# Kernel tuning notes

Measured on AMD Instinct MI355X. Metric: run time of the kernel, lower is better.

Reference implementation:

```python
import jax, jax.numpy as jnp
import numpy as np

N_NODES = 100000
N_EDGES = 1600000
IN_DIM = 64
OUT_DIM = 64
HIDDEN = 64  # fixed in edge_weight_mlp
POS_DIM = 3


def setup_inputs() -> dict:
    key = jax.random.key(0)
    ks = jax.random.split(key, 10)
    x = jax.random.normal(ks[0], (N_NODES, IN_DIM), dtype=jnp.float32)
    edge_index = jax.random.randint(ks[1], (2, N_EDGES), 0, N_NODES, dtype=jnp.int64)
    pos = jax.random.normal(ks[2], (N_NODES, POS_DIM), dtype=jnp.float32)
    # edge_weight_mlp params: Linear(2*IN_DIM+1 -> 64), Linear(64 -> 1)
    s1 = 1.0 / np.sqrt(2 * IN_DIM + 1)
    w1 = jax.random.uniform(ks[3], (2 * IN_DIM + 1, HIDDEN), jnp.float32, -s1, s1)
    b1 = jax.random.uniform(ks[4], (HIDDEN,), jnp.float32, -s1, s1)
    s2 = 1.0 / np.sqrt(HIDDEN)
    w2 = jax.random.uniform(ks[5], (HIDDEN, 1), jnp.float32, -s2, s2)
    b2 = jax.random.uniform(ks[6], (1,), jnp.float32, -s2, s2)
    # transform: Linear(IN_DIM -> OUT_DIM)
    st = 1.0 / np.sqrt(IN_DIM)
    wt = jax.random.uniform(ks[7], (IN_DIM, OUT_DIM), jnp.float32, -st, st)
    bt = jax.random.uniform(ks[8], (OUT_DIM,), jnp.float32, -st, st)
    return {"x": x, "edge_index": edge_index, "pos": pos,
            "w1": w1, "b1": b1, "w2": w2, "b2": b2, "wt": wt, "bt": bt}


def reference(x, edge_index, pos, w1, b1, w2, b2, wt, bt):
    src, dst = edge_index[0], edge_index[1]
    # edge weights: MLP on [x_src, x_dst, |pos_dst - pos_src|]
    edge_length = jnp.linalg.norm(pos[dst] - pos[src], axis=1, keepdims=True)  # [E,1]
    edge_feat = jnp.concatenate([x[src], x[dst], edge_length], axis=1)  # [E, 2*in+1]
    h = jax.nn.relu(edge_feat @ w1 + b1)
    edge_weights = jax.nn.sigmoid(h @ w2 + b2)  # [E,1]
    # node transform, gather, weight, scatter-add
    x_t = x @ wt + bt  # [N, out]
    messages = x_t[src] * edge_weights  # [E, out]
    out = jax.ops.segment_sum(messages, dst, num_segments=x.shape[0])  # [N, out]
    return out, edge_weights
```

## Files before the change

kernel.cpp:

```cpp
#include <hip/hip_runtime.h>
#include <hip/hip_bf16.h>
#include <math.h>

#define NN 100000
#define NE 1600000
#define CAP 48
#define NB 391
#define BCAP 4608
#define EPB 4096
#define NBLKA ((NE + EPB - 1) / EPB)
#define NPREP ((NN + 63) / 64)
#define PSTR 72

typedef __attribute__((ext_vector_type(8))) short short8;
typedef __attribute__((ext_vector_type(4))) float floatx4;

static __device__ __forceinline__ unsigned short f2bb(float f) {
    __hip_bfloat16 h = __float2bfloat16(f);
    return *(unsigned short*)&h;
}
static __device__ __forceinline__ float hi_f(unsigned u) {
    return __uint_as_float(u & 0xFFFF0000u);
}
static __device__ __forceinline__ float lo_f(unsigned u) {
    return __uint_as_float(u << 16);
}

__global__ __launch_bounds__(256) void fused_prep_bucket(
    const float* __restrict__ x, const float* __restrict__ w1,
    const float* __restrict__ b1, const float* __restrict__ pos,
    const int* __restrict__ ei,
    unsigned int* __restrict__ rec, unsigned short* __restrict__ hd,
    float4* __restrict__ pos4, int* __restrict__ gcursor,
    uint2* __restrict__ bucketed) {
    __shared__ __align__(16) unsigned char smem[(64 + 128) * PSTR * 2];
    int t = threadIdx.x;
    if (blockIdx.x < NPREP) {
        unsigned short* As = (unsigned short*)smem;
        unsigned short* Bs = As + 64 * PSTR;
        int nbase = blockIdx.x * 64;
        {
            int r = t & 63;
            int node = nbase + r; if (node >= NN) node = NN - 1;
            const float4* xr = (const float4*)(x + (size_t)node * 64);
#pragma unroll
            for (int i = 0; i < 4; ++i) {
                int s = (t >> 6) + 4 * i;
                float4 v = xr[s];
                ushort4 o = {f2bb(v.x), f2bb(v.y), f2bb(v.z), f2bb(v.w)};
                *(ushort4*)&As[r * PSTR + s * 4] = o;
            }
        }
        {
            int n = t & 127;
            int kh = t >> 7;
            int krow = (n < 64) ? 0 : 64;
            int col = n & 63;
#pragma unroll
            for (int i = 0; i < 32; ++i) {
                int k = kh * 32 + i;
                Bs[n * PSTR + k] = f2bb(w1[(krow + k) * 64 + col]);
            }
        }
        if (t < 64) {
            int node = nbase + t;
            if (node < NN)
                pos4[node] = make_float4(pos[node * 3 + 0], pos[node * 3 + 1],
                                         pos[node * 3 + 2], 0.f);
        }
        __syncthreads();
        int lane = t & 63, wave = t >> 6;
        int grp = lane >> 4, l15 = lane & 15;
        floatx4 acc[8] = {};
        int arow = wave * 16 + l15;
#pragma unroll
        for (int ks = 0; ks < 2; ++ks) {
            int koff = ks * 32 + grp * 8;
            short8 a = *(const short8*)&As[arow * PSTR + koff];
#pragma unroll
            for (int nt = 0; nt < 8; ++nt) {
                short8 b = *(const short8*)&Bs[(nt * 16 + l15) * PSTR + koff];
                acc[nt] = __builtin_amdgcn_mfma_f32_16x16x32_bf16(a, b, acc[nt], 0, 0, 0);
            }
        }
#pragma unroll
        for (int nt = 0; nt < 8; ++nt) {
#pragma unroll
            for (int r = 0; r < 4; ++r) {
                int nr = wave * 16 + grp * 4 + r;
                int node = nbase + nr;
                if (node >= NN) continue;
                if (nt < 4) {
                    int col = nt * 16 + l15;
                    unsigned xbits = As[nr * PSTR + col];
                    rec[(size_t)node * 64 + col] =
                        ((unsigned)f2bb(acc[nt][r]) << 16) | xbits;
                } else {
                    int col = (nt - 4) * 16 + l15;
                    hd[(size_t)node * 64 + col] = f2bb(acc[nt][r] + b1[col]);
                }
            }
        }
    } else {
        int* cnt = (int*)smem;
        int* base_s = cnt + NB;
        for (int i = t; i < NB; i += 256) cnt[i] = 0;
        __syncthreads();
        int e0 = (blockIdx.x - NPREP) * EPB;
        unsigned int tags[16];
        int srcs[16], dsts[16];
#pragma unroll
        for (int i = 0; i < 16; ++i) {
            int e = e0 + i * 256 + t;
            tags[i] = 0xFFFFFFFFu;
            if (e < NE) {
                srcs[i] = ei[e];
                dsts[i] = ei[NE + e];
                int b = dsts[i] >> 8;
                int slot = atomicAdd(&cnt[b], 1);
                tags[i] = ((unsigned)b << 12) | (unsigned)slot;
            }
        }
        __syncthreads();
        for (int b = t; b < NB; b += 256)
            base_s[b] = atomicAdd(&gcursor[b], cnt[b]);
        __syncthreads();
#pragma unroll
        for (int i = 0; i < 16; ++i) {
            if (tags[i] != 0xFFFFFFFFu) {
                int e = e0 + i * 256 + t;
                int b = (int)(tags[i] >> 12);
                int slot = (int)(tags[i] & 0xFFFu);
                int p = base_s[b] + slot;
                if (p < BCAP) {
                    bucketed[(size_t)b * BCAP + p] =
                        make_uint2((unsigned)srcs[i] |
                                   (((unsigned)dsts[i] & 255u) << 17),
                                   (unsigned)e);
                }
            }
        }
    }
}

__global__ __launch_bounds__(1024) void csr_kernel(
    const uint2* __restrict__ bucketed, const int* __restrict__ gcursor,
    uint2* __restrict__ pairs, int* __restrict__ deg) {
    __shared__ int cur[256];
    int t = threadIdx.x;
    if (t < 256) cur[t] = 0;
    __syncthreads();
    int b = blockIdx.x;
    int n0 = b << 8;
    int cnt = gcursor[b];
    if (cnt > BCAP) cnt = BCAP;
    for (int i = t; i < cnt; i += 1024) {
        uint2 en = bucketed[(size_t)b * BCAP + i];
        int dwb = (int)((en.x >> 17) & 255u);
        unsigned src = en.x & 0x1FFFFu;
        int slot = atomicAdd(&cur[dwb], 1);
        if (slot < CAP)
            pairs[(size_t)(n0 + dwb) * CAP + slot] = make_uint2(src, en.y);
    }
    __syncthreads();
    if (t < 256) {
        int node = n0 + t;
        if (node < NN) deg[node] = (cur[t] > CAP) ? CAP : cur[t];
    }
}

__global__ __launch_bounds__(256) void mega_kernel(
    const uint2* __restrict__ pairs, const int* __restrict__ deg,
    const unsigned int* __restrict__ rec, const unsigned short* __restrict__ hd,
    const float4* __restrict__ pos4, const float* __restrict__ w1,
    const float* __restrict__ w2, const float* __restrict__ b2,
    float* __restrict__ ew_out, unsigned short* __restrict__ aggb,
    float* __restrict__ sumw) {
    int t = threadIdx.x;
    int w = t >> 6, lane = t & 63;
    int e8 = lane >> 3, hg = lane & 7;
    int node = blockIdx.x * 4 + w;
    if (node >= NN) return;

    float acc0 = 0.f, acc1 = 0.f, acc2 = 0.f, acc3 = 0.f;
    float acc4 = 0.f, acc5 = 0.f, acc6 = 0.f, acc7 = 0.f, sw = 0.f;
    int d = deg[node];
    uint4 hz = ((const uint4*)(hd + (size_t)node * 64))[hg];
    float zb0 = lo_f(hz.x), zb1 = hi_f(hz.x);
    float zb2 = lo_f(hz.y), zb3 = hi_f(hz.y);
    float zb4 = lo_f(hz.z), zb5 = hi_f(hz.z);
    float zb6 = lo_f(hz.w), zb7 = hi_f(hz.w);
    float4 w2a = ((const float4*)w2)[2 * hg];
    float4 w2b = ((const float4*)w2)[2 * hg + 1];
    float4 wla = ((const float4*)(w1 + 128 * 64))[2 * hg];
    float4 wlb = ((const float4*)(w1 + 128 * 64))[2 * hg + 1];
    float4 pd = pos4[node];
    float b2v = b2[0];
    const uint2* seg = pairs + (size_t)node * CAP;
    const uint4* rec4 = (const uint4*)rec;

    if (d > 0) {
        int i0 = (e8 < d) ? e8 : (d - 1);
        uint2 pr_c = seg[i0];
        uint2 pr_n = pr_c;
        if (8 < d) { int i1 = (8 + e8 < d) ? (8 + e8) : (d - 1); pr_n = seg[i1]; }
        uint4 ua_c = rec4[(size_t)pr_c.x * 16 + 2 * hg];
        uint4 ub_c = rec4[(size_t)pr_c.x * 16 + 2 * hg + 1];
        float4 ps_c = pos4[pr_c.x];

        for (int j = 0; j < d; j += 8) {
            int jn = j + 8;
            uint2 pr_n2 = pr_n;
            uint4 ua_n = ua_c, ub_n = ub_c;
            float4 ps_n = ps_c;
            if (jn < d) {
                ua_n = rec4[(size_t)pr_n.x * 16 + 2 * hg];
                ub_n = rec4[(size_t)pr_n.x * 16 + 2 * hg + 1];
                ps_n = pos4[pr_n.x];
                if (jn + 8 < d) {
                    int i2 = (jn + 8 + e8 < d) ? (jn + 8 + e8) : (d - 1);
                    pr_n2 = seg[i2];
                }
            }
            bool valid = (j + e8 < d);
            float dx = pd.x - ps_c.x;
            float dy = pd.y - ps_c.y;
            float dz = pd.z - ps_c.z;
            float len = __builtin_amdgcn_sqrtf(dx * dx + dy * dy + dz * dz);

            float tt;
            {
                float z0 = zb0 + hi_f(ua_c.x) + len * wla.x;
                float z1 = zb1 + hi_f(ua_c.y) + len * wla.y;
                float z2 = zb2 + hi_f(ua_c.z) + len * wla.z;
                float z3 = zb3 + hi_f(ua_c.w) + len * wla.w;
                float z4 = zb4 + hi_f(ub_c.x) + len * wlb.x;
                float z5 = zb5 + hi_f(ub_c.y) + len * wlb.y;
                float z6 = zb6 + hi_f(ub_c.z) + len * wlb.z;
                float z7 = zb7 + hi_f(ub_c.w) + len * wlb.w;
                tt = fmaxf(z0, 0.f) * w2a.x;
                tt = fmaf(fmaxf(z1, 0.f), w2a.y, tt);
                tt = fmaf(fmaxf(z2, 0.f), w2a.z, tt);
                tt = fmaf(fmaxf(z3, 0.f), w2a.w, tt);
                tt = fmaf(fmaxf(z4, 0.f), w2b.x, tt);
                tt = fmaf(fmaxf(z5, 0.f), w2b.y, tt);
                tt = fmaf(fmaxf(z6, 0.f), w2b.z, tt);
                tt = fmaf(fmaxf(z7, 0.f), w2b.w, tt);
            }
            tt += __shfl_xor(tt, 1);
            tt += __shfl_xor(tt, 2);
            tt += __shfl_xor(tt, 4);
            float ew = __builtin_amdgcn_rcpf(1.f + __expf(-(tt + b2v)));
            if (valid) {
                if (hg == 0) ew_out[pr_c.y] = ew;
                acc0 = fmaf(ew, lo_f(ua_c.x), acc0);
                acc1 = fmaf(ew, lo_f(ua_c.y), acc1);
                acc2 = fmaf(ew, lo_f(ua_c.z), acc2);
                acc3 = fmaf(ew, lo_f(ua_c.w), acc3);
                acc4 = fmaf(ew, lo_f(ub_c.x), acc4);
                acc5 = fmaf(ew, lo_f(ub_c.y), acc5);
                acc6 = fmaf(ew, lo_f(ub_c.z), acc6);
                acc7 = fmaf(ew, lo_f(ub_c.w), acc7);
                sw += ew;
            }
            pr_c = pr_n; pr_n = pr_n2;
            ua_c = ua_n; ub_c = ub_n; ps_c = ps_n;
        }
    }
#pragma unroll
    for (int off = 8; off < 64; off <<= 1) {
        acc0 += __shfl_xor(acc0, off);
        acc1 += __shfl_xor(acc1, off);
        acc2 += __shfl_xor(acc2, off);
        acc3 += __shfl_xor(acc3, off);
        acc4 += __shfl_xor(acc4, off);
        acc5 += __shfl_xor(acc5, off);
        acc6 += __shfl_xor(acc6, off);
        acc7 += __shfl_xor(acc7, off);
        sw   += __shfl_xor(sw, off);
    }
    if (e8 == 0) {
        uint4 o;
        o.x = ((unsigned)f2bb(acc1) << 16) | f2bb(acc0);
        o.y = ((unsigned)f2bb(acc3) << 16) | f2bb(acc2);
        o.z = ((unsigned)f2bb(acc5) << 16) | f2bb(acc4);
        o.w = ((unsigned)f2bb(acc7) << 16) | f2bb(acc6);
        *(uint4*)(aggb + (size_t)node * 64 + hg * 8) = o;
    }
    if (lane == 0) sumw[node] = sw;
}

__global__ __launch_bounds__(256) void transform_mfma(
    const unsigned short* __restrict__ aggb, const float* __restrict__ sumw,
    const float* __restrict__ wt, const float* __restrict__ bt,
    float* __restrict__ out) {
    __shared__ unsigned short As[64 * PSTR];
    __shared__ unsigned short Bs[64 * PSTR];
    int t = threadIdx.x;
    int nbase = blockIdx.x * 64;
    {
        int r = t & 63;
        int node = nbase + r; if (node >= NN) node = NN - 1;
        const uint4* ar = (const uint4*)(aggb + (size_t)node * 64);
#pragma unroll
        for (int i = 0; i < 2; ++i) {
            int s = (t >> 6) + 4 * i;
            *(uint4*)&As[r * PSTR + s * 8] = ar[s];
        }
    }
    {
        int n = t & 63;
        int kq = t >> 6;
#pragma unroll
        for (int i = 0; i < 16; ++i) {
            int k = kq * 16 + i;
            Bs[n * PSTR + k] = f2bb(wt[k * 64 + n]);
        }
    }
    __syncthreads();
    int lane = t & 63, wave = t >> 6;
    int grp = lane >> 4, l15 = lane & 15;
    floatx4 acc[4] = {};
    int arow = wave * 16 + l15;
#pragma unroll
    for (int ks = 0; ks < 2; ++ks) {
        int koff = ks * 32 + grp * 8;
        short8 a = *(const short8*)&As[arow * PSTR + koff];
#pragma unroll
        for (int nt = 0; nt < 4; ++nt) {
            short8 b = *(const short8*)&Bs[(nt * 16 + l15) * PSTR + koff];
            acc[nt] = __builtin_amdgcn_mfma_f32_16x16x32_bf16(a, b, acc[nt], 0, 0, 0);
        }
    }
#pragma unroll
    for (int nt = 0; nt < 4; ++nt) {
        int col = nt * 16 + l15;
        float btv = bt[col];
#pragma unroll
        for (int r = 0; r < 4; ++r) {
            int node = nbase + wave * 16 + grp * 4 + r;
            if (node < NN)
                out[(size_t)node * 64 + col] = acc[nt][r] + sumw[node] * btv;
        }
    }
}

extern "C" void kernel_launch(void* const* d_in, const int* in_sizes, int n_in,
                              void* d_out, int out_size, void* d_ws, size_t ws_size,
                              hipStream_t stream) {
    const float* x   = (const float*)d_in[0];
    const int*   ei  = (const int*)d_in[1];
    const float* pos = (const float*)d_in[2];
    const float* w1  = (const float*)d_in[3];
    const float* b1  = (const float*)d_in[4];
    const float* w2  = (const float*)d_in[5];
    const float* b2  = (const float*)d_in[6];
    const float* wt  = (const float*)d_in[7];
    const float* bt  = (const float*)d_in[8];

    float* out    = (float*)d_out;
    float* ew_out = out + (size_t)NN * 64;

    unsigned int* rec = (unsigned int*)d_ws;
    unsigned short* hd = (unsigned short*)(rec + (size_t)NN * 64);
    uint2* pairs = (uint2*)(hd + (size_t)NN * 64);
    unsigned short* aggb = (unsigned short*)(pairs + (size_t)NN * CAP);
    float4* pos4 = (float4*)(aggb + (size_t)NN * 64);
    float* sumw = (float*)(pos4 + NN);
    int* gcursor = (int*)(sumw + NN);
    int* deg = gcursor + NB;

    uint2* bucketed = (uint2*)d_out;

    hipMemsetAsync(gcursor, 0, NB * sizeof(int), stream);
    fused_prep_bucket<<<NPREP + NBLKA, 256, 0, stream>>>(
        x, w1, b1, pos, ei, rec, hd, pos4, gcursor, bucketed);
    csr_kernel<<<NB, 1024, 0, stream>>>(bucketed, gcursor, pairs, deg);
    mega_kernel<<<(NN + 3) / 4, 256, 0, stream>>>(pairs, deg, rec, hd, pos4,
                                                  w1, w2, b2, ew_out, aggb, sumw);
    transform_mfma<<<(NN + 63) / 64, 256, 0, stream>>>(aggb, sumw, wt, bt, out);
}
```

Measured before the change: 244.7 us.

## Fuse node transform MFMA into aggregation kernel via shared memory

Merges the separate transform_mfma kernel into mega_kernel. Each block now processes 16 nodes (4 per wave, serially), stages the bf16 aggregates and weight sums in LDS, then runs a 16x64 MFMA tile per block and writes the output directly. This removes the global round trip of aggb and sumw plus one kernel launch. In exchange, every block re-converts the full wt matrix into LDS, which is 6250 times instead of about 1563. It also adds a block barrier and lowers node-level parallelism per wave.

```diff
diff --git a/kernel.cpp b/kernel.cpp
--- a/kernel.cpp
+++ b/kernel.cpp
@@ -174,174 +174,156 @@
     const unsigned int* __restrict__ rec, const unsigned short* __restrict__ hd,
     const float4* __restrict__ pos4, const float* __restrict__ w1,
     const float* __restrict__ w2, const float* __restrict__ b2,
-    float* __restrict__ ew_out, unsigned short* __restrict__ aggb,
-    float* __restrict__ sumw) {
+    const float* __restrict__ wt, const float* __restrict__ bt,
+    float* __restrict__ ew_out, float* __restrict__ out) {
+    __shared__ __align__(16) unsigned short Bs[64 * PSTR];
+    __shared__ __align__(16) unsigned short agg_s[16 * PSTR];
+    __shared__ float sumw_s[16];
     int t = threadIdx.x;
     int w = t >> 6, lane = t & 63;
     int e8 = lane >> 3, hg = lane & 7;
-    int node = blockIdx.x * 4 + w;
-    if (node >= NN) return;
-
-    float acc0 = 0.f, acc1 = 0.f, acc2 = 0.f, acc3 = 0.f;
-    float acc4 = 0.f, acc5 = 0.f, acc6 = 0.f, acc7 = 0.f, sw = 0.f;
-    int d = deg[node];
-    uint4 hz = ((const uint4*)(hd + (size_t)node * 64))[hg];
-    float zb0 = lo_f(hz.x), zb1 = hi_f(hz.x);
-    float zb2 = lo_f(hz.y), zb3 = hi_f(hz.y);
-    float zb4 = lo_f(hz.z), zb5 = hi_f(hz.z);
-    float zb6 = lo_f(hz.w), zb7 = hi_f(hz.w);
+    int nbase = blockIdx.x * 16;
+
+    {
+        int n = t & 63;
+        int kq = t >> 6;
+#pragma unroll
+        for (int i = 0; i < 16; ++i) {
+            int k = kq * 16 + i;
+            Bs[n * PSTR + k] = f2bb(wt[k * 64 + n]);
+        }
+    }
+
     float4 w2a = ((const float4*)w2)[2 * hg];
     float4 w2b = ((const float4*)w2)[2 * hg + 1];
     float4 wla = ((const float4*)(w1 + 128 * 64))[2 * hg];
     float4 wlb = ((const float4*)(w1 + 128 * 64))[2 * hg + 1];
-    float4 pd = pos4[node];
     float b2v = b2[0];
-    const uint2* seg = pairs + (size_t)node * CAP;
     const uint4* rec4 = (const uint4*)rec;
 
-    if (d > 0) {
-        int i0 = (e8 < d) ? e8 : (d - 1);
-        uint2 pr_c = seg[i0];
-        uint2 pr_n = pr_c;
-        if (8 < d) { int i1 = (8 + e8 < d) ? (8 + e8) : (d - 1); pr_n = seg[i1]; }
-        uint4 ua_c = rec4[(size_t)pr_c.x * 16 + 2 * hg];
-        uint4 ub_c = rec4[(size_t)pr_c.x * 16 + 2 * hg + 1];
-        float4 ps_c = pos4[pr_c.x];
-
-        for (int j = 0; j < d; j += 8) {
-            int jn = j + 8;
-            uint2 pr_n2 = pr_n;
-            uint4 ua_n = ua_c, ub_n = ub_c;
-            float4 ps_n = ps_c;
-            if (jn < d) {
-                ua_n = rec4[(size_t)pr_n.x * 16 + 2 * hg];
-                ub_n = rec4[(size_t)pr_n.x * 16 + 2 * hg + 1];
-                ps_n = pos4[pr_n.x];
-                if (jn + 8 < d) {
-                    int i2 = (jn + 8 + e8 < d) ? (jn + 8 + e8) : (d - 1);
-                    pr_n2 = seg[i2];
+#pragma unroll 1
+    for (int i = 0; i < 4; ++i) {
+        int node_l = w * 4 + i;
+        int node = nbase + node_l;
+        float acc0 = 0.f, acc1 = 0.f, acc2 = 0.f, acc3 = 0.f;
+        float acc4 = 0.f, acc5 = 0.f, acc6 = 0.f, acc7 = 0.f, sw = 0.f;
+        if (node < NN) {
+            int d = deg[node];
+            uint4 hz = ((const uint4*)(hd + (size_t)node * 64))[hg];
+            float zb0 = lo_f(hz.x), zb1 = hi_f(hz.x);
+            float zb2 = lo_f(hz.y), zb3 = hi_f(hz.y);
+            float zb4 = lo_f(hz.z), zb5 = hi_f(hz.z);
+            float zb6 = lo_f(hz.w), zb7 = hi_f(hz.w);
+            float4 pd = pos4[node];
+            const uint2* seg = pairs + (size_t)node * CAP;
+
+            if (d > 0) {
+                int i0 = (e8 < d) ? e8 : (d - 1);
+                uint2 pr_c = seg[i0];
+                uint2 pr_n = pr_c;
+                if (8 < d) { int i1 = (8 + e8 < d) ? (8 + e8) : (d - 1); pr_n = seg[i1]; }
+                uint4 ua_c = rec4[(size_t)pr_c.x * 16 + 2 * hg];
+                uint4 ub_c = rec4[(size_t)pr_c.x * 16 + 2 * hg + 1];
+                float4 ps_c = pos4[pr_c.x];
+
+                for (int j = 0; j < d; j += 8) {
+                    int jn = j + 8;
+                    uint2 pr_n2 = pr_n;
+                    uint4 ua_n = ua_c, ub_n = ub_c;
+                    float4 ps_n = ps_c;
+                    if (jn < d) {
+                        ua_n = rec4[(size_t)pr_n.x * 16 + 2 * hg];
+                        ub_n = rec4[(size_t)pr_n.x * 16 + 2 * hg + 1];
+                        ps_n = pos4[pr_n.x];
+                        if (jn + 8 < d) {
+                            int i2 = (jn + 8 + e8 < d) ? (jn + 8 + e8) : (d - 1);
+                            pr_n2 = seg[i2];
+                        }
+                    }
+                    bool valid = (j + e8 < d);
+                    float dx = pd.x - ps_c.x;
+                    float dy = pd.y - ps_c.y;
+                    float dz = pd.z - ps_c.z;
+                    float len = __builtin_amdgcn_sqrtf(dx * dx + dy * dy + dz * dz);
+
+                    float z0 = zb0 + hi_f(ua_c.x) + len * wla.x;
+                    float z1 = zb1 + hi_f(ua_c.y) + len * wla.y;
+                    float z2 = zb2 + hi_f(ua_c.z) + len * wla.z;
+                    float z3 = zb3 + hi_f(ua_c.w) + len * wla.w;
+                    float z4 = zb4 + hi_f(ub_c.x) + len * wlb.x;
+                    float z5 = zb5 + hi_f(ub_c.y) + len * wlb.y;
+                    float z6 = zb6 + hi_f(ub_c.z) + len * wlb.z;
+                    float z7 = zb7 + hi_f(ub_c.w) + len * wlb.w;
+                    float tt = fmaxf(z0, 0.f) * w2a.x;
+                    tt = fmaf(fmaxf(z1, 0.f), w2a.y, tt);
+                    tt = fmaf(fmaxf(z2, 0.f), w2a.z, tt);
+                    tt = fmaf(fmaxf(z3, 0.f), w2a.w, tt);
+                    tt = fmaf(fmaxf(z4, 0.f), w2b.x, tt);
+                    tt = fmaf(fmaxf(z5, 0.f), w2b.y, tt);
+                    tt = fmaf(fmaxf(z6, 0.f), w2b.z, tt);
+                    tt = fmaf(fmaxf(z7, 0.f), w2b.w, tt);
+                    tt += __shfl_xor(tt, 1);
+                    tt += __shfl_xor(tt, 2);
+                    tt += __shfl_xor(tt, 4);
+                    float ew = __builtin_amdgcn_rcpf(1.f + __expf(-(tt + b2v)));
+                    if (valid) {
+                        if (hg == 0) ew_out[pr_c.y] = ew;
+                        acc0 = fmaf(ew, lo_f(ua_c.x), acc0);
+                        acc1 = fmaf(ew, lo_f(ua_c.y), acc1);
+                        acc2 = fmaf(ew, lo_f(ua_c.z), acc2);
+                        acc3 = fmaf(ew, lo_f(ua_c.w), acc3);
+                        acc4 = fmaf(ew, lo_f(ub_c.x), acc4);
+                        acc5 = fmaf(ew, lo_f(ub_c.y), acc5);
+                        acc6 = fmaf(ew, lo_f(ub_c.z), acc6);
+                        acc7 = fmaf(ew, lo_f(ub_c.w), acc7);
+                        sw += ew;
+                    }
+                    pr_c = pr_n; pr_n = pr_n2;
+                    ua_c = ua_n; ub_c = ub_n; ps_c = ps_n;
                 }
             }
-            bool valid = (j + e8 < d);
-            float dx = pd.x - ps_c.x;
-            float dy = pd.y - ps_c.y;
-            float dz = pd.z - ps_c.z;
-            float len = __builtin_amdgcn_sqrtf(dx * dx + dy * dy + dz * dz);
-
-            float tt;
-            {
-                float z0 = zb0 + hi_f(ua_c.x) + len * wla.x;
-                float z1 = zb1 + hi_f(ua_c.y) + len * wla.y;
-                float z2 = zb2 + hi_f(ua_c.z) + len * wla.z;
-                float z3 = zb3 + hi_f(ua_c.w) + len * wla.w;
-                float z4 = zb4 + hi_f(ub_c.x) + len * wlb.x;
-                float z5 = zb5 + hi_f(ub_c.y) + len * wlb.y;
-                float z6 = zb6 + hi_f(ub_c.z) + len * wlb.z;
-                float z7 = zb7 + hi_f(ub_c.w) + len * wlb.w;
-                tt = fmaxf(z0, 0.f) * w2a.x;
-                tt = fmaf(fmaxf(z1, 0.f), w2a.y, tt);
-                tt = fmaf(fmaxf(z2, 0.f), w2a.z, tt);
-                tt = fmaf(fmaxf(z3, 0.f), w2a.w, tt);
-                tt = fmaf(fmaxf(z4, 0.f), w2b.x, tt);
-                tt = fmaf(fmaxf(z5, 0.f), w2b.y, tt);
-                tt = fmaf(fmaxf(z6, 0.f), w2b.z, tt);
-                tt = fmaf(fmaxf(z7, 0.f), w2b.w, tt);
-            }
-            tt += __shfl_xor(tt, 1);
-            tt += __shfl_xor(tt, 2);
-            tt += __shfl_xor(tt, 4);
-            float ew = __builtin_amdgcn_rcpf(1.f + __expf(-(tt + b2v)));
-            if (valid) {
-                if (hg == 0) ew_out[pr_c.y] = ew;
-                acc0 = fmaf(ew, lo_f(ua_c.x), acc0);
-                acc1 = fmaf(ew, lo_f(ua_c.y), acc1);
-                acc2 = fmaf(ew, lo_f(ua_c.z), acc2);
-                acc3 = fmaf(ew, lo_f(ua_c.w), acc3);
-                acc4 = fmaf(ew, lo_f(ub_c.x), acc4);
-                acc5 = fmaf(ew, lo_f(ub_c.y), acc5);
-                acc6 = fmaf(ew, lo_f(ub_c.z), acc6);
-                acc7 = fmaf(ew, lo_f(ub_c.w), acc7);
-                sw += ew;
-            }
-            pr_c = pr_n; pr_n = pr_n2;
-            ua_c = ua_n; ub_c = ub_n; ps_c = ps_n;
-        }
-    }
-#pragma unroll
-    for (int off = 8; off < 64; off <<= 1) {
-        acc0 += __shfl_xor(acc0, off);
-        acc1 += __shfl_xor(acc1, off);
-        acc2 += __shfl_xor(acc2, off);
-        acc3 += __shfl_xor(acc3, off);
-        acc4 += __shfl_xor(acc4, off);
-        acc5 += __shfl_xor(acc5, off);
-        acc6 += __shfl_xor(acc6, off);
-        acc7 += __shfl_xor(acc7, off);
-        sw   += __shfl_xor(sw, off);
-    }
-    if (e8 == 0) {
-        uint4 o;
-        o.x = ((unsigned)f2bb(acc1) << 16) | f2bb(acc0);
-        o.y = ((unsigned)f2bb(acc3) << 16) | f2bb(acc2);
-        o.z = ((unsigned)f2bb(acc5) << 16) | f2bb(acc4);
-        o.w = ((unsigned)f2bb(acc7) << 16) | f2bb(acc6);
-        *(uint4*)(aggb + (size_t)node * 64 + hg * 8) = o;
-    }
-    if (lane == 0) sumw[node] = sw;
-}
-
-__global__ __launch_bounds__(256) void transform_mfma(
-    const unsigned short* __restrict__ aggb, const float* __restrict__ sumw,
-    const float* __restrict__ wt, const float* __restrict__ bt,
-    float* __restrict__ out) {
-    __shared__ unsigned short As[64 * PSTR];
-    __shared__ unsigned short Bs[64 * PSTR];
-    int t = threadIdx.x;
-    int nbase = blockIdx.x * 64;
-    {
-        int r = t & 63;
-        int node = nbase + r; if (node >= NN) node = NN - 1;
-        const uint4* ar = (const uint4*)(aggb + (size_t)node * 64);
-#pragma unroll
-        for (int i = 0; i < 2; ++i) {
-            int s = (t >> 6) + 4 * i;
-            *(uint4*)&As[r * PSTR + s * 8] = ar[s];
-        }
-    }
-    {
-        int n = t & 63;
-        int kq = t >> 6;
-#pragma unroll
-        for (int i = 0; i < 16; ++i) {
-            int k = kq * 16 + i;
-            Bs[n * PSTR + k] = f2bb(wt[k * 64 + n]);
-        }
+        }
+#pragma unroll
+        for (int off = 8; off < 64; off <<= 1) {
+            acc0 += __shfl_xor(acc0, off);
+            acc1 += __shfl_xor(acc1, off);
+            acc2 += __shfl_xor(acc2, off);
+            acc3 += __shfl_xor(acc3, off);
+            acc4 += __shfl_xor(acc4, off);
+            acc5 += __shfl_xor(acc5, off);
+            acc6 += __shfl_xor(acc6, off);
+            acc7 += __shfl_xor(acc7, off);
+            sw   += __shfl_xor(sw, off);
+        }
+        if (e8 == 0) {
+            uint4 o;
+            o.x = ((unsigned)f2bb(acc1) << 16) | f2bb(acc0);
+            o.y = ((unsigned)f2bb(acc3) << 16) | f2bb(acc2);
+            o.z = ((unsigned)f2bb(acc5) << 16) | f2bb(acc4);
+            o.w = ((unsigned)f2bb(acc7) << 16) | f2bb(acc6);
+            *(uint4*)&agg_s[node_l * PSTR + hg * 8] = o;
+        }
+        if (lane == 0) sumw_s[node_l] = sw;
     }
     __syncthreads();
-    int lane = t & 63, wave = t >> 6;
+
     int grp = lane >> 4, l15 = lane & 15;
-    floatx4 acc[4] = {};
-    int arow = wave * 16 + l15;
+    floatx4 acc = {};
 #pragma unroll
     for (int ks = 0; ks < 2; ++ks) {
         int koff = ks * 32 + grp * 8;
-        short8 a = *(const short8*)&As[arow * PSTR + koff];
-#pragma unroll
-        for (int nt = 0; nt < 4; ++nt) {
-            short8 b = *(const short8*)&Bs[(nt * 16 + l15) * PSTR + koff];
-            acc[nt] = __builtin_amdgcn_mfma_f32_16x16x32_bf16(a, b, acc[nt], 0, 0, 0);
-        }
-    }
-#pragma unroll
-    for (int nt = 0; nt < 4; ++nt) {
-        int col = nt * 16 + l15;
-        float btv = bt[col];
-#pragma unroll
-        for (int r = 0; r < 4; ++r) {
-            int node = nbase + wave * 16 + grp * 4 + r;
-            if (node < NN)
-                out[(size_t)node * 64 + col] = acc[nt][r] + sumw[node] * btv;
-        }
+        short8 a = *(const short8*)&agg_s[l15 * PSTR + koff];
+        short8 b = *(const short8*)&Bs[(w * 16 + l15) * PSTR + koff];
+        acc = __builtin_amdgcn_mfma_f32_16x16x32_bf16(a, b, acc, 0, 0, 0);
+    }
+    int col = w * 16 + l15;
+    float btv = bt[col];
+#pragma unroll
+    for (int r = 0; r < 4; ++r) {
+        int row = grp * 4 + r;
+        int node = nbase + row;
+        if (node < NN)
+            out[(size_t)node * 64 + col] = acc[r] + sumw_s[row] * btv;
     }
 }
 
@@ -364,10 +346,8 @@
     unsigned int* rec = (unsigned int*)d_ws;
     unsigned short* hd = (unsigned short*)(rec + (size_t)NN * 64);
     uint2* pairs = (uint2*)(hd + (size_t)NN * 64);
-    unsigned short* aggb = (unsigned short*)(pairs + (size_t)NN * CAP);
-    float4* pos4 = (float4*)(aggb + (size_t)NN * 64);
-    float* sumw = (float*)(pos4 + NN);
-    int* gcursor = (int*)(sumw + NN);
+    float4* pos4 = (float4*)(pairs + (size_t)NN * CAP);
+    int* gcursor = (int*)(pos4 + NN);
     int* deg = gcursor + NB;
 
     uint2* bucketed = (uint2*)d_out;
@@ -376,7 +356,6 @@
     fused_prep_bucket<<<NPREP + NBLKA, 256, 0, stream>>>(
         x, w1, b1, pos, ei, rec, hd, pos4, gcursor, bucketed);
     csr_kernel<<<NB, 1024, 0, stream>>>(bucketed, gcursor, pairs, deg);
-    mega_kernel<<<(NN + 3) / 4, 256, 0, stream>>>(pairs, deg, rec, hd, pos4,
-                                                  w1, w2, b2, ew_out, aggb, sumw);
-    transform_mfma<<<(NN + 63) / 64, 256, 0, stream>>>(aggb, sumw, wt, bt, out);
-}
+    mega_kernel<<<(NN + 15) / 16, 256, 0, stream>>>(pairs, deg, rec, hd, pos4,
+                                                    w1, w2, b2, wt, bt, ew_out, out);
+}
```

Result: no change. 248.7 us (+1.6%).

## Fuse CSR build and per-node edge MLP aggregation into one kernel

Applied to the files above, without the earlier changes.

Merges the CSR bucket-to-pairs kernel and the per-node edge MLP/aggregation kernel into one launch. Each 1024-thread block builds the adjacency lists for its 256 nodes, reads node degrees from shared memory, and then has each of its 16 waves process 16 nodes sequentially. This removes a launch and the global deg array, and the pairs it just wrote are likely still in cache. In exchange, parallelism drops to 391 blocks with serial per-wave node loops, which may underfill the GPU and leave latency exposed. The LDS padding stride in the transform kernel also changes from 72 to 68.

```diff
diff --git a/kernel.cpp b/kernel.cpp
--- a/kernel.cpp
+++ b/kernel.cpp
@@ -10,7 +10,7 @@
 #define EPB 4096
 #define NBLKA ((NE + EPB - 1) / EPB)
 #define NPREP ((NN + 63) / 64)
-#define PSTR 72
+#define PSTR 68
 
 typedef __attribute__((ext_vector_type(8))) short short8;
 typedef __attribute__((ext_vector_type(4))) float floatx4;
@@ -143,15 +143,20 @@
     }
 }
 
-__global__ __launch_bounds__(1024) void csr_kernel(
+__global__ __launch_bounds__(1024) void csr_mega(
     const uint2* __restrict__ bucketed, const int* __restrict__ gcursor,
-    uint2* __restrict__ pairs, int* __restrict__ deg) {
+    uint2* __restrict__ pairs,
+    const unsigned int* __restrict__ rec, const unsigned short* __restrict__ hd,
+    const float4* __restrict__ pos4, const float* __restrict__ w1,
+    const float* __restrict__ w2, const float* __restrict__ b2,
+    float* __restrict__ ew_out, unsigned short* __restrict__ aggb,
+    float* __restrict__ sumw) {
     __shared__ int cur[256];
     int t = threadIdx.x;
+    int b = blockIdx.x;
+    int n0 = b << 8;
     if (t < 256) cur[t] = 0;
     __syncthreads();
-    int b = blockIdx.x;
-    int n0 = b << 8;
     int cnt = gcursor[b];
     if (cnt > BCAP) cnt = BCAP;
     for (int i = t; i < cnt; i += 1024) {
@@ -162,74 +167,64 @@
         if (slot < CAP)
             pairs[(size_t)(n0 + dwb) * CAP + slot] = make_uint2(src, en.y);
     }
+    __threadfence_block();
     __syncthreads();
-    if (t < 256) {
-        int node = n0 + t;
-        if (node < NN) deg[node] = (cur[t] > CAP) ? CAP : cur[t];
-    }
-}
-
-__global__ __launch_bounds__(256) void mega_kernel(
-    const uint2* __restrict__ pairs, const int* __restrict__ deg,
-    const unsigned int* __restrict__ rec, const unsigned short* __restrict__ hd,
-    const float4* __restrict__ pos4, const float* __restrict__ w1,
-    const float* __restrict__ w2, const float* __restrict__ b2,
-    float* __restrict__ ew_out, unsigned short* __restrict__ aggb,
-    float* __restrict__ sumw) {
-    int t = threadIdx.x;
-    int w = t >> 6, lane = t & 63;
+
+    int wv = t >> 6, lane = t & 63;
     int e8 = lane >> 3, hg = lane & 7;
-    int node = blockIdx.x * 4 + w;
-    if (node >= NN) return;
-
-    float acc0 = 0.f, acc1 = 0.f, acc2 = 0.f, acc3 = 0.f;
-    float acc4 = 0.f, acc5 = 0.f, acc6 = 0.f, acc7 = 0.f, sw = 0.f;
-    int d = deg[node];
-    uint4 hz = ((const uint4*)(hd + (size_t)node * 64))[hg];
-    float zb0 = lo_f(hz.x), zb1 = hi_f(hz.x);
-    float zb2 = lo_f(hz.y), zb3 = hi_f(hz.y);
-    float zb4 = lo_f(hz.z), zb5 = hi_f(hz.z);
-    float zb6 = lo_f(hz.w), zb7 = hi_f(hz.w);
     float4 w2a = ((const float4*)w2)[2 * hg];
     float4 w2b = ((const float4*)w2)[2 * hg + 1];
     float4 wla = ((const float4*)(w1 + 128 * 64))[2 * hg];
     float4 wlb = ((const float4*)(w1 + 128 * 64))[2 * hg + 1];
-    float4 pd = pos4[node];
     float b2v = b2[0];
-    const uint2* seg = pairs + (size_t)node * CAP;
     const uint4* rec4 = (const uint4*)rec;
 
-    if (d > 0) {
-        int i0 = (e8 < d) ? e8 : (d - 1);
-        uint2 pr_c = seg[i0];
-        uint2 pr_n = pr_c;
-        if (8 < d) { int i1 = (8 + e8 < d) ? (8 + e8) : (d - 1); pr_n = seg[i1]; }
-        uint4 ua_c = rec4[(size_t)pr_c.x * 16 + 2 * hg];
-        uint4 ub_c = rec4[(size_t)pr_c.x * 16 + 2 * hg + 1];
-        float4 ps_c = pos4[pr_c.x];
-
-        for (int j = 0; j < d; j += 8) {
-            int jn = j + 8;
-            uint2 pr_n2 = pr_n;
-            uint4 ua_n = ua_c, ub_n = ub_c;
-            float4 ps_n = ps_c;
-            if (jn < d) {
-                ua_n = rec4[(size_t)pr_n.x * 16 + 2 * hg];
-                ub_n = rec4[(size_t)pr_n.x * 16 + 2 * hg + 1];
-                ps_n = pos4[pr_n.x];
-                if (jn + 8 < d) {
-                    int i2 = (jn + 8 + e8 < d) ? (jn + 8 + e8) : (d - 1);
-                    pr_n2 = seg[i2];
+#pragma unroll 1
+    for (int i = 0; i < 16; ++i) {
+        int node_l = wv * 16 + i;
+        int node = n0 + node_l;
+        if (node >= NN) break;
+        int d = cur[node_l];
+        if (d > CAP) d = CAP;
+        float acc0 = 0.f, acc1 = 0.f, acc2 = 0.f, acc3 = 0.f;
+        float acc4 = 0.f, acc5 = 0.f, acc6 = 0.f, acc7 = 0.f, sw = 0.f;
+        uint4 hz = ((const uint4*)(hd + (size_t)node * 64))[hg];
+        float zb0 = lo_f(hz.x), zb1 = hi_f(hz.x);
+        float zb2 = lo_f(hz.y), zb3 = hi_f(hz.y);
+        float zb4 = lo_f(hz.z), zb5 = hi_f(hz.z);
+        float zb6 = lo_f(hz.w), zb7 = hi_f(hz.w);
+        float4 pd = pos4[node];
+        const uint2* seg = pairs + (size_t)node * CAP;
+
+        if (d > 0) {
+            int i0 = (e8 < d) ? e8 : (d - 1);
+            uint2 pr_c = seg[i0];
+            uint2 pr_n = pr_c;
+            if (8 < d) { int i1 = (8 + e8 < d) ? (8 + e8) : (d - 1); pr_n = seg[i1]; }
+            uint4 ua_c = rec4[(size_t)pr_c.x * 16 + 2 * hg];
+            uint4 ub_c = rec4[(size_t)pr_c.x * 16 + 2 * hg + 1];
+            float4 ps_c = pos4[pr_c.x];
+
+            for (int j = 0; j < d; j += 8) {
+                int jn = j + 8;
+                uint2 pr_n2 = pr_n;
+                uint4 ua_n = ua_c, ub_n = ub_c;
+                float4 ps_n = ps_c;
+                if (jn < d) {
+                    ua_n = rec4[(size_t)pr_n.x * 16 + 2 * hg];
+                    ub_n = rec4[(size_t)pr_n.x * 16 + 2 * hg + 1];
+                    ps_n = pos4[pr_n.x];
+                    if (jn + 8 < d) {
+                        int i2 = (jn + 8 + e8 < d) ? (jn + 8 + e8) : (d - 1);
+                        pr_n2 = seg[i2];
+                    }
                 }
-            }
-            bool valid = (j + e8 < d);
-            float dx = pd.x - ps_c.x;
-            float dy = pd.y - ps_c.y;
-            float dz = pd.z - ps_c.z;
-            float len = __builtin_amdgcn_sqrtf(dx * dx + dy * dy + dz * dz);
-
-            float tt;
-            {
+                bool valid = (j + e8 < d);
+                float dx = pd.x - ps_c.x;
+                float dy = pd.y - ps_c.y;
+                float dz = pd.z - ps_c.z;
+                float len = __builtin_amdgcn_sqrtf(dx * dx + dy * dy + dz * dz);
+
                 float z0 = zb0 + hi_f(ua_c.x) + len * wla.x;
                 float z1 = zb1 + hi_f(ua_c.y) + len * wla.y;
                 float z2 = zb2 + hi_f(ua_c.z) + len * wla.z;
@@ -238,7 +233,7 @@
                 float z5 = zb5 + hi_f(ub_c.y) + len * wlb.y;
                 float z6 = zb6 + hi_f(ub_c.z) + len * wlb.z;
                 float z7 = zb7 + hi_f(ub_c.w) + len * wlb.w;
-                tt = fmaxf(z0, 0.f) * w2a.x;
+                float tt = fmaxf(z0, 0.f) * w2a.x;
                 tt = fmaf(fmaxf(z1, 0.f), w2a.y, tt);
                 tt = fmaf(fmaxf(z2, 0.f), w2a.z, tt);
                 tt = fmaf(fmaxf(z3, 0.f), w2a.w, tt);
@@ -246,48 +241,48 @@
                 tt = fmaf(fmaxf(z5, 0.f), w2b.y, tt);
                 tt = fmaf(fmaxf(z6, 0.f), w2b.z, tt);
                 tt = fmaf(fmaxf(z7, 0.f), w2b.w, tt);
-            }
-            tt += __shfl_xor(tt, 1);
-            tt += __shfl_xor(tt, 2);
-            tt += __shfl_xor(tt, 4);
-            float ew = __builtin_amdgcn_rcpf(1.f + __expf(-(tt + b2v)));
-            if (valid) {
-                if (hg == 0) ew_out[pr_c.y] = ew;
-                acc0 = fmaf(ew, lo_f(ua_c.x), acc0);
-                acc1 = fmaf(ew, lo_f(ua_c.y), acc1);
-                acc2 = fmaf(ew, lo_f(ua_c.z), acc2);
-                acc3 = fmaf(ew, lo_f(ua_c.w), acc3);
-                acc4 = fmaf(ew, lo_f(ub_c.x), acc4);
-                acc5 = fmaf(ew, lo_f(ub_c.y), acc5);
-                acc6 = fmaf(ew, lo_f(ub_c.z), acc6);
-                acc7 = fmaf(ew, lo_f(ub_c.w), acc7);
-                sw += ew;
-            }
-            pr_c = pr_n; pr_n = pr_n2;
-            ua_c = ua_n; ub_c = ub_n; ps_c = ps_n;
-        }
-    }
-#pragma unroll
-    for (int off = 8; off < 64; off <<= 1) {
-        acc0 += __shfl_xor(acc0, off);
-        acc1 += __shfl_xor(acc1, off);
-        acc2 += __shfl_xor(acc2, off);
-        acc3 += __shfl_xor(acc3, off);
-        acc4 += __shfl_xor(acc4, off);
-        acc5 += __shfl_xor(acc5, off);
-        acc6 += __shfl_xor(acc6, off);
-        acc7 += __shfl_xor(acc7, off);
-        sw   += __shfl_xor(sw, off);
-    }
-    if (e8 == 0) {
-        uint4 o;
-        o.x = ((unsigned)f2bb(acc1) << 16) | f2bb(acc0);
-        o.y = ((unsigned)f2bb(acc3) << 16) | f2bb(acc2);
-        o.z = ((unsigned)f2bb(acc5) << 16) | f2bb(acc4);
-        o.w = ((unsigned)f2bb(acc7) << 16) | f2bb(acc6);
-        *(uint4*)(aggb + (size_t)node * 64 + hg * 8) = o;
-    }
-    if (lane == 0) sumw[node] = sw;
+                tt += __shfl_xor(tt, 1);
+                tt += __shfl_xor(tt, 2);
+                tt += __shfl_xor(tt, 4);
+                float ew = __builtin_amdgcn_rcpf(1.f + __expf(-(tt + b2v)));
+                if (valid) {
+                    if (hg == 0) ew_out[pr_c.y] = ew;
+                    acc0 = fmaf(ew, lo_f(ua_c.x), acc0);
+                    acc1 = fmaf(ew, lo_f(ua_c.y), acc1);
+                    acc2 = fmaf(ew, lo_f(ua_c.z), acc2);
+                    acc3 = fmaf(ew, lo_f(ua_c.w), acc3);
+                    acc4 = fmaf(ew, lo_f(ub_c.x), acc4);
+                    acc5 = fmaf(ew, lo_f(ub_c.y), acc5);
+                    acc6 = fmaf(ew, lo_f(ub_c.z), acc6);
+                    acc7 = fmaf(ew, lo_f(ub_c.w), acc7);
+                    sw += ew;
+                }
+                pr_c = pr_n; pr_n = pr_n2;
+                ua_c = ua_n; ub_c = ub_n; ps_c = ps_n;
+            }
+        }
+#pragma unroll
+        for (int off = 8; off < 64; off <<= 1) {
+            acc0 += __shfl_xor(acc0, off);
+            acc1 += __shfl_xor(acc1, off);
+            acc2 += __shfl_xor(acc2, off);
+            acc3 += __shfl_xor(acc3, off);
+            acc4 += __shfl_xor(acc4, off);
+            acc5 += __shfl_xor(acc5, off);
+            acc6 += __shfl_xor(acc6, off);
+            acc7 += __shfl_xor(acc7, off);
+            sw   += __shfl_xor(sw, off);
+        }
+        if (e8 == 0) {
+            uint4 o;
+            o.x = ((unsigned)f2bb(acc1) << 16) | f2bb(acc0);
+            o.y = ((unsigned)f2bb(acc3) << 16) | f2bb(acc2);
+            o.z = ((unsigned)f2bb(acc5) << 16) | f2bb(acc4);
+            o.w = ((unsigned)f2bb(acc7) << 16) | f2bb(acc6);
+            *(uint4*)(aggb + (size_t)node * 64 + hg * 8) = o;
+        }
+        if (lane == 0) sumw[node] = sw;
+    }
 }
 
 __global__ __launch_bounds__(256) void transform_mfma(
@@ -368,15 +363,13 @@
     float4* pos4 = (float4*)(aggb + (size_t)NN * 64);
     float* sumw = (float*)(pos4 + NN);
     int* gcursor = (int*)(sumw + NN);
-    int* deg = gcursor + NB;
 
     uint2* bucketed = (uint2*)d_out;
 
     hipMemsetAsync(gcursor, 0, NB * sizeof(int), stream);
     fused_prep_bucket<<<NPREP + NBLKA, 256, 0, stream>>>(
         x, w1, b1, pos, ei, rec, hd, pos4, gcursor, bucketed);
-    csr_kernel<<<NB, 1024, 0, stream>>>(bucketed, gcursor, pairs, deg);
-    mega_kernel<<<(NN + 3) / 4, 256, 0, stream>>>(pairs, deg, rec, hd, pos4,
-                                                  w1, w2, b2, ew_out, aggb, sumw);
+    csr_mega<<<NB, 1024, 0, stream>>>(bucketed, gcursor, pairs, rec, hd, pos4,
+                                      w1, w2, b2, ew_out, aggb, sumw);
     transform_mfma<<<(NN + 63) / 64, 256, 0, stream>>>(aggb, sumw, wt, bt, out);
 }
```

After: 265.5 us. 8.5% more time.
